# Optimization experiments

Measured on AMD Instinct MI355X. Metric: run time of the kernel, lower is better.

Reference implementation:

```python
import jax, jax.numpy as jnp
import numpy as np

P, N, M = 4, 8192, 8192

def setup_inputs() -> dict:
    key = jax.random.key(0)
    k1, k2, k3, k4, k5 = jax.random.split(key, 5)
    return {
        "camera_pts": jax.random.normal(k1, (P, N, 3), dtype=jnp.float32),
        "cad_pts": jax.random.normal(k2, (P, M, 3), dtype=jnp.float32),
        "part_weight": jax.random.uniform(k3, (P,), dtype=jnp.float32),
        "rot_quat": jax.random.normal(k4, (P, 4), dtype=jnp.float32),
        "tra": jax.random.normal(k5, (P, 3, 1), dtype=jnp.float32),
    }

def _quat_to_rot(q):
    # q: [P,4] in (w,x,y,z) order, normalized outside
    a, b, c, d = q[:, 0], q[:, 1], q[:, 2], q[:, 3]
    rows = jnp.stack([
        1 - 2*c*c - 2*d*d, 2*b*c - 2*a*d,     2*a*c + 2*b*d,
        2*b*c + 2*a*d,     1 - 2*b*b - 2*d*d, 2*c*d - 2*a*b,
        2*b*d - 2*a*c,     2*a*b + 2*c*d,     1 - 2*b*b - 2*c*c,
    ], axis=-1)  # [P,9]
    return rows.reshape(-1, 3, 3)

def _chamfer(x, y):
    # x: [N,4], y: [M,4] -> scalar bidirectional chamfer (Euclidean, not squared)
    x2 = jnp.sum(x * x, axis=-1)              # [N]
    y2 = jnp.sum(y * y, axis=-1)              # [M]
    d2 = x2[:, None] + y2[None, :] - 2.0 * (x @ y.T)
    dist = jnp.sqrt(jnp.clip(d2, 0.0))        # [N,M]
    return jnp.mean(jnp.min(dist, axis=1)) + jnp.mean(jnp.min(dist, axis=0))

def reference(camera_pts, cad_pts, part_weight, rot_quat, tra):
    q = rot_quat / jnp.linalg.norm(rot_quat, axis=1, keepdims=True)
    rot = _quat_to_rot(q)                                       # [P,3,3]
    top = jnp.concatenate([rot, tra], axis=2)                   # [P,3,4]
    bottom = jnp.broadcast_to(jnp.array([[[0.0, 0.0, 0.0, 1.0]]], dtype=rot.dtype), (rot.shape[0], 1, 4))
    transforms = jnp.concatenate([top, bottom], axis=1)         # [P,4,4]
    ones_cad = jnp.ones(cad_pts.shape[:-1] + (1,), dtype=cad_pts.dtype)
    ones_cam = jnp.ones(camera_pts.shape[:-1] + (1,), dtype=camera_pts.dtype)
    cad_h = jnp.concatenate([cad_pts, ones_cad], axis=-1)       # [P,M,4]
    cam_h = jnp.concatenate([camera_pts, ones_cam], axis=-1)    # [P,N,4]
    cad_base = jnp.einsum('pij,pmj->pmi', transforms, cad_h)    # [P,M,4]
    cd = jax.vmap(_chamfer)(cad_base, cam_h)                    # [P]
    all_objective = jnp.sum(part_weight * cd)
    return all_objective, jax.lax.stop_gradient(transforms)
```

## Files before the change

### kernel.cpp

```cpp
#include <hip/hip_runtime.h>
#include <math.h>

#define NP 4
#define NN 8192
#define NM 8192

#define PK_A_F4 0
#define PK_B_F4 (NP * NM)
#define MINS_OFF ((NP * NM + NP * NN) * 4)
#define MINB_REL (NP * NM)

#define TQ 16
#define QT 4096
#define SPLITS 64
#define SPAN 128

#define RED_BLOCKS 128

__device__ inline float min3f(float a, float b, float c) {
    float d;
    asm("v_min3_f32 %0, %1, %2, %3" : "=v"(d) : "v"(a), "v"(b), "v"(c));
    return d;
}

__device__ inline void make_transform(const float* __restrict__ quat,
                                      const float* __restrict__ tra,
                                      int p, float T[12]) {
    float q0 = quat[p * 4 + 0], q1 = quat[p * 4 + 1];
    float q2 = quat[p * 4 + 2], q3 = quat[p * 4 + 3];
    float inv = 1.0f / sqrtf(q0 * q0 + q1 * q1 + q2 * q2 + q3 * q3);
    float a = q0 * inv, b = q1 * inv, c = q2 * inv, d = q3 * inv;
    T[0] = 1.0f - 2.0f * c * c - 2.0f * d * d;
    T[1] = 2.0f * b * c - 2.0f * a * d;
    T[2] = 2.0f * a * c + 2.0f * b * d;
    T[3] = tra[p * 3 + 0];
    T[4] = 2.0f * b * c + 2.0f * a * d;
    T[5] = 1.0f - 2.0f * b * b - 2.0f * d * d;
    T[6] = 2.0f * c * d - 2.0f * a * b;
    T[7] = tra[p * 3 + 1];
    T[8] = 2.0f * b * d - 2.0f * a * c;
    T[9] = 2.0f * a * b + 2.0f * c * d;
    T[10] = 1.0f - 2.0f * b * b - 2.0f * c * c;
    T[11] = tra[p * 3 + 2];
}

__global__ __launch_bounds__(256) void prep_kernel(
    const float* __restrict__ cam, const float* __restrict__ cad,
    const float* __restrict__ quat, const float* __restrict__ tra,
    float* __restrict__ ws, float* __restrict__ out) {
    int idx = blockIdx.x * 256 + threadIdx.x;
    const float INF = __uint_as_float(0x7f800000u);

    if (idx < NP * NM) {
        int p = idx >> 13;
        int m = idx & (NM - 1);
        float T[12];
        make_transform(quat, tra, p, T);
        float x = cad[(p * NM + m) * 3 + 0];
        float y = cad[(p * NM + m) * 3 + 1];
        float z = cad[(p * NM + m) * 3 + 2];
        float vx = fmaf(T[0], x, fmaf(T[1], y, fmaf(T[2], z, T[3])));
        float vy = fmaf(T[4], x, fmaf(T[5], y, fmaf(T[6], z, T[7])));
        float vz = fmaf(T[8], x, fmaf(T[9], y, fmaf(T[10], z, T[11])));
        float h = 0.5f * (vx * vx + vy * vy + vz * vz);
        ((float4*)ws)[PK_A_F4 + idx] = make_float4(vx, vy, vz, h);
        ws[MINS_OFF + idx] = INF;
    } else {
        int k = idx - NP * NM;
        float vx = cam[k * 3 + 0];
        float vy = cam[k * 3 + 1];
        float vz = cam[k * 3 + 2];
        float h = 0.5f * (vx * vx + vy * vy + vz * vz);
        ((float4*)ws)[PK_B_F4 + k] = make_float4(vx, vy, vz, h);
        ws[MINS_OFF + MINB_REL + k] = INF;
    }

    if (idx < 64) {
        int p2 = idx >> 4;
        int r = (idx >> 2) & 3;
        int c = idx & 3;
        float T[12];
        make_transform(quat, tra, p2, T);
        float v;
        if (r == 3)
            v = (c == 3) ? 1.0f : 0.0f;
        else
            v = T[r * 4 + c];
        out[1 + idx] = v;
    } else if (idx == 64) {
        out[0] = 0.0f;
    }
}

__global__ __launch_bounds__(256, 2) void chamfer_kernel(
    const float4* __restrict__ packed, float* __restrict__ mins) {
    int tid = threadIdx.x;
    int p = blockIdx.z >> 1;
    int role = blockIdx.z & 1;

    const float4* Q;
    const float4* T;
    float* minarr;
    if (role == 0) {
        Q = packed + PK_A_F4 + p * NM;
        T = packed + PK_B_F4 + p * NN;
        minarr = mins + p * NM;
    } else {
        Q = packed + PK_B_F4 + p * NN;
        T = packed + PK_A_F4 + p * NM;
        minarr = mins + MINB_REL + p * NN;
    }

    __shared__ float4 sT[SPAN];

    const float INF = __uint_as_float(0x7f800000u);
    int q0 = blockIdx.x * QT + tid;
    float qx[TQ], qy[TQ], qz[TQ], qw[TQ], tmin[TQ];
#pragma unroll
    for (int k = 0; k < TQ; ++k) {
        float4 v = Q[q0 + k * 256];
        qx[k] = v.x; qy[k] = v.y; qz[k] = v.z; qw[k] = v.w;
        tmin[k] = INF;
    }

    int tbase = blockIdx.y * SPAN;
    for (int j = tid; j < SPAN; j += 256) sT[j] = T[tbase + j];
    __syncthreads();

#pragma unroll 2
    for (int j = 0; j < SPAN; j += 2) {
        float4 t0 = sT[j];
        float4 t1 = sT[j + 1];
#pragma unroll
        for (int k = 0; k < TQ; ++k) {
            float s0 = fmaf(-qx[k], t0.x, fmaf(-qy[k], t0.y, fmaf(-qz[k], t0.z, t0.w)));
            float s1 = fmaf(-qx[k], t1.x, fmaf(-qy[k], t1.y, fmaf(-qz[k], t1.z, t1.w)));
            tmin[k] = min3f(tmin[k], s0, s1);
        }
    }

#pragma unroll
    for (int k = 0; k < TQ; ++k) {
        float d2 = 2.0f * (qw[k] + tmin[k]);
        d2 = fmaxf(d2, 0.0f);
        atomicMin((unsigned int*)&minarr[q0 + k * 256], __float_as_uint(d2));
    }
}

__global__ __launch_bounds__(256) void finalize_kernel(
    const float* __restrict__ ws, const float* __restrict__ w,
    float* __restrict__ out) {
    const float* vals = ws + MINS_OFF;
    int i = blockIdx.x * 256 + threadIdx.x;
    int tid = threadIdx.x;

    float wl[4] = {w[0], w[1], w[2], w[3]};

    int i2 = i + 32768;
    float acc = wl[(i >> 13) & 3] * sqrtf(vals[i]) +
                wl[(i2 >> 13) & 3] * sqrtf(vals[i2]);

#pragma unroll
    for (int off = 32; off > 0; off >>= 1) acc += __shfl_down(acc, off, 64);

    __shared__ float wsum[4];
    if ((tid & 63) == 0) wsum[tid >> 6] = acc;
    __syncthreads();
    if (tid == 0) {
        float blocksum = (wsum[0] + wsum[1] + wsum[2] + wsum[3]) * (1.0f / 8192.0f);
        atomicAdd(out, blocksum);
    }
}

extern "C" void kernel_launch(void* const* d_in, const int* in_sizes, int n_in,
                              void* d_out, int out_size, void* d_ws, size_t ws_size,
                              hipStream_t stream) {
    const float* cam = (const float*)d_in[0];
    const float* cad = (const float*)d_in[1];
    const float* w = (const float*)d_in[2];
    const float* quat = (const float*)d_in[3];
    const float* tra = (const float*)d_in[4];
    float* out = (float*)d_out;
    float* ws = (float*)d_ws;

    prep_kernel<<<(NP * (NM + NN)) / 256, 256, 0, stream>>>(cam, cad, quat, tra, ws, out);

    dim3 grid(NM / QT, SPLITS, 2 * NP);
    chamfer_kernel<<<grid, 256, 0, stream>>>((const float4*)ws, ws + MINS_OFF);

    finalize_kernel<<<RED_BLOCKS, 256, 0, stream>>>(ws, w, out);
}
```

Measured before the change: 109.3 us.

## Use packed FP32 FMA with pair-interleaved target layout in chamfer kernel

Prep now also writes target points in a pair-interleaved SoA layout (x0x1,y0y1,z0z1,h0h1), so the chamfer inner loop can evaluate two targets per v_pk_fma_f32 and halve FMA instruction count. Queries per thread drop from 16 to 8 with more blocks, and launch bounds move to a waves-per-eu hint for higher occupancy. Shared-memory reads are software-prefetched one pair ahead. The risk is extra prep writes and larger grid/atomic traffic, plus relying on packed-math throughput.

```diff
diff --git a/kernel.cpp b/kernel.cpp
--- a/kernel.cpp
+++ b/kernel.cpp
@@ -5,21 +5,30 @@
 #define NN 8192
 #define NM 8192
 
-#define PK_A_F4 0
-#define PK_B_F4 (NP * NM)
-#define MINS_OFF ((NP * NM + NP * NN) * 4)
+#define PKA_OFF 0
+#define PKB_OFF 131072
+#define PRA_OFF 262144
+#define PRB_OFF 393216
+#define MINS_OFF 524288
 #define MINB_REL (NP * NM)
 
-#define TQ 16
-#define QT 4096
+#define TQ 8
+#define QT 2048
 #define SPLITS 64
 #define SPAN 128
 
-#define RED_BLOCKS 128
+typedef float float2v __attribute__((ext_vector_type(2)));
+typedef float float4v __attribute__((ext_vector_type(4)));
 
 __device__ inline float min3f(float a, float b, float c) {
     float d;
     asm("v_min3_f32 %0, %1, %2, %3" : "=v"(d) : "v"(a), "v"(b), "v"(c));
+    return d;
+}
+
+__device__ inline float2v pk_fma(float2v a, float2v b, float2v c) {
+    float2v d;
+    asm("v_pk_fma_f32 %0, %1, %2, %3" : "=v"(d) : "v"(a), "v"(b), "v"(c));
     return d;
 }
 
@@ -51,29 +60,40 @@
     int idx = blockIdx.x * 256 + threadIdx.x;
     const float INF = __uint_as_float(0x7f800000u);
 
+    float vx, vy, vz;
+    int pkoff, proff, local;
     if (idx < NP * NM) {
         int p = idx >> 13;
-        int m = idx & (NM - 1);
         float T[12];
         make_transform(quat, tra, p, T);
-        float x = cad[(p * NM + m) * 3 + 0];
-        float y = cad[(p * NM + m) * 3 + 1];
-        float z = cad[(p * NM + m) * 3 + 2];
-        float vx = fmaf(T[0], x, fmaf(T[1], y, fmaf(T[2], z, T[3])));
-        float vy = fmaf(T[4], x, fmaf(T[5], y, fmaf(T[6], z, T[7])));
-        float vz = fmaf(T[8], x, fmaf(T[9], y, fmaf(T[10], z, T[11])));
-        float h = 0.5f * (vx * vx + vy * vy + vz * vz);
-        ((float4*)ws)[PK_A_F4 + idx] = make_float4(vx, vy, vz, h);
-        ws[MINS_OFF + idx] = INF;
+        float x = cad[idx * 3 + 0];
+        float y = cad[idx * 3 + 1];
+        float z = cad[idx * 3 + 2];
+        vx = fmaf(T[0], x, fmaf(T[1], y, fmaf(T[2], z, T[3])));
+        vy = fmaf(T[4], x, fmaf(T[5], y, fmaf(T[6], z, T[7])));
+        vz = fmaf(T[8], x, fmaf(T[9], y, fmaf(T[10], z, T[11])));
+        pkoff = PKA_OFF;
+        proff = PRA_OFF;
+        local = idx;
     } else {
         int k = idx - NP * NM;
-        float vx = cam[k * 3 + 0];
-        float vy = cam[k * 3 + 1];
-        float vz = cam[k * 3 + 2];
-        float h = 0.5f * (vx * vx + vy * vy + vz * vz);
-        ((float4*)ws)[PK_B_F4 + k] = make_float4(vx, vy, vz, h);
-        ws[MINS_OFF + MINB_REL + k] = INF;
-    }
+        vx = cam[k * 3 + 0];
+        vy = cam[k * 3 + 1];
+        vz = cam[k * 3 + 2];
+        pkoff = PKB_OFF;
+        proff = PRB_OFF;
+        local = k;
+    }
+    float h = 0.5f * (vx * vx + vy * vy + vz * vz);
+    ((float4*)(ws + pkoff))[local] = make_float4(vx, vy, vz, h);
+    int lane = local & 1;
+    size_t f = (size_t)proff + (size_t)(local & ~1) * 4;
+    ws[f + lane] = vx;
+    ws[f + 2 + lane] = vy;
+    ws[f + 4 + lane] = vz;
+    ws[f + 6 + lane] = h;
+
+    ws[MINS_OFF + idx] = INF;
 
     if (idx < 64) {
         int p2 = idx >> 4;
@@ -92,51 +112,64 @@
     }
 }
 
-__global__ __launch_bounds__(256, 2) void chamfer_kernel(
-    const float4* __restrict__ packed, float* __restrict__ mins) {
+__global__ __launch_bounds__(256)
+__attribute__((amdgpu_waves_per_eu(2, 4)))
+void chamfer_kernel(const float* __restrict__ ws, float* __restrict__ mins) {
     int tid = threadIdx.x;
     int p = blockIdx.z >> 1;
     int role = blockIdx.z & 1;
 
     const float4* Q;
-    const float4* T;
+    const float4v* T;
     float* minarr;
     if (role == 0) {
-        Q = packed + PK_A_F4 + p * NM;
-        T = packed + PK_B_F4 + p * NN;
+        Q = (const float4*)(ws + PKA_OFF) + p * NM;
+        T = (const float4v*)(ws + PRB_OFF) + p * NN;
         minarr = mins + p * NM;
     } else {
-        Q = packed + PK_B_F4 + p * NN;
-        T = packed + PK_A_F4 + p * NM;
+        Q = (const float4*)(ws + PKB_OFF) + p * NN;
+        T = (const float4v*)(ws + PRA_OFF) + p * NM;
         minarr = mins + MINB_REL + p * NN;
     }
 
-    __shared__ float4 sT[SPAN];
+    __shared__ float4v sQd[SPAN];
 
     const float INF = __uint_as_float(0x7f800000u);
     int q0 = blockIdx.x * QT + tid;
-    float qx[TQ], qy[TQ], qz[TQ], qw[TQ], tmin[TQ];
+    float2v nqx[TQ], nqy[TQ], nqz[TQ];
+    float qw[TQ], tmin[TQ];
 #pragma unroll
     for (int k = 0; k < TQ; ++k) {
         float4 v = Q[q0 + k * 256];
-        qx[k] = v.x; qy[k] = v.y; qz[k] = v.z; qw[k] = v.w;
+        nqx[k] = (float2v){-v.x, -v.x};
+        nqy[k] = (float2v){-v.y, -v.y};
+        nqz[k] = (float2v){-v.z, -v.z};
+        qw[k] = v.w;
         tmin[k] = INF;
     }
 
     int tbase = blockIdx.y * SPAN;
-    for (int j = tid; j < SPAN; j += 256) sT[j] = T[tbase + j];
+    if (tid < SPAN) sQd[tid] = T[tbase + tid];
     __syncthreads();
 
+    float4v cXY = sQd[0], cZH = sQd[1];
 #pragma unroll 2
-    for (int j = 0; j < SPAN; j += 2) {
-        float4 t0 = sT[j];
-        float4 t1 = sT[j + 1];
+    for (int pp = 0; pp < SPAN / 2; ++pp) {
+        int pn = (pp + 1) & (SPAN / 2 - 1);
+        float4v nXY = sQd[2 * pn];
+        float4v nZH = sQd[2 * pn + 1];
+
+        float2v X = __builtin_shufflevector(cXY, cXY, 0, 1);
+        float2v Y = __builtin_shufflevector(cXY, cXY, 2, 3);
+        float2v Z = __builtin_shufflevector(cZH, cZH, 0, 1);
+        float2v H = __builtin_shufflevector(cZH, cZH, 2, 3);
 #pragma unroll
         for (int k = 0; k < TQ; ++k) {
-            float s0 = fmaf(-qx[k], t0.x, fmaf(-qy[k], t0.y, fmaf(-qz[k], t0.z, t0.w)));
-            float s1 = fmaf(-qx[k], t1.x, fmaf(-qy[k], t1.y, fmaf(-qz[k], t1.z, t1.w)));
-            tmin[k] = min3f(tmin[k], s0, s1);
+            float2v s = pk_fma(nqx[k], X, pk_fma(nqy[k], Y, pk_fma(nqz[k], Z, H)));
+            tmin[k] = min3f(tmin[k], s.x, s.y);
         }
+        cXY = nXY;
+        cZH = nZH;
     }
 
 #pragma unroll
@@ -183,10 +216,10 @@
     float* out = (float*)d_out;
     float* ws = (float*)d_ws;
 
-    prep_kernel<<<(NP * (NM + NN)) / 256, 256, 0, stream>>>(cam, cad, quat, tra, ws, out);
+    prep_kernel<<<256, 256, 0, stream>>>(cam, cad, quat, tra, ws, out);
 
     dim3 grid(NM / QT, SPLITS, 2 * NP);
-    chamfer_kernel<<<grid, 256, 0, stream>>>((const float4*)ws, ws + MINS_OFF);
-
-    finalize_kernel<<<RED_BLOCKS, 256, 0, stream>>>(ws, w, out);
-}
+    chamfer_kernel<<<grid, 256, 0, stream>>>(ws, ws + MINS_OFF);
+
+    finalize_kernel<<<128, 256, 0, stream>>>(ws, w, out);
+}
```

New measurement: 104.8 us. -4.1%, faster.

## Compute both chamfer directions in one pass with packed FMA and DPP reductions

Applied to the files above, without the earlier changes.

Replaces the two-role chamfer pass, which evaluated every distance twice, with a single pass per point pair that updates both the per-camera-point minimum in registers and the per-CAD-point minimum via a wave-level DPP min reduction. The prep kernel is fused into the chamfer kernel, and the global atomicMin is replaced by partial-minimum buffers that the finalize kernel reduces. Distance evaluation uses v_pk_fma_f32 on pairs of target points, and a bias term folds the second half-norm in with a single packed add. The cost is extra DPP/readlane work for each query point, a larger workspace for the partial minima, and a heavier finalize reduction over 64 slices.

```diff
diff --git a/kernel.cpp b/kernel.cpp
--- a/kernel.cpp
+++ b/kernel.cpp
@@ -5,23 +5,38 @@
 #define NN 8192
 #define NM 8192
 
-#define PK_A_F4 0
-#define PK_B_F4 (NP * NM)
-#define MINS_OFF ((NP * NM + NP * NN) * 4)
-#define MINB_REL (NP * NM)
-
-#define TQ 16
-#define QT 4096
-#define SPLITS 64
-#define SPAN 128
-
-#define RED_BLOCKS 128
+#define QS 64
+#define QB 128
+#define TS 2
+#define TT 16
+#define SLAB 4096
+
+#define BIAS 1024.0f
+
+#define PA_OFF 0
+#define PB_OFF (TS * NP * NM)
+
+typedef float float2v __attribute__((ext_vector_type(2)));
 
 __device__ inline float min3f(float a, float b, float c) {
     float d;
     asm("v_min3_f32 %0, %1, %2, %3" : "=v"(d) : "v"(a), "v"(b), "v"(c));
     return d;
 }
+__device__ inline float2v pk_fma(float2v a, float2v b, float2v c) {
+    float2v d;
+    asm("v_pk_fma_f32 %0, %1, %2, %3" : "=v"(d) : "v"(a), "v"(b), "v"(c));
+    return d;
+}
+__device__ inline float2v pk_add(float2v a, float2v b) {
+    float2v d;
+    asm("v_pk_add_f32 %0, %1, %2" : "=v"(d) : "v"(a), "v"(b));
+    return d;
+}
+
+#define DPP_MIN(r, ctrl)                                                     \
+    r = fminf(r, __uint_as_float((unsigned)__builtin_amdgcn_update_dpp(      \
+                     0, (int)__float_as_uint(r), (ctrl), 0xf, 0xf, true)))
 
 __device__ inline void make_transform(const float* __restrict__ quat,
                                       const float* __restrict__ tra,
@@ -44,121 +59,117 @@
     T[11] = tra[p * 3 + 2];
 }
 
-__global__ __launch_bounds__(256) void prep_kernel(
+__global__ __launch_bounds__(256, 2) void chamfer_kernel(
     const float* __restrict__ cam, const float* __restrict__ cad,
     const float* __restrict__ quat, const float* __restrict__ tra,
     float* __restrict__ ws, float* __restrict__ out) {
-    int idx = blockIdx.x * 256 + threadIdx.x;
+    int tid = threadIdx.x;
+    int lane = tid & 63;
+    int wv = tid >> 6;
+    int qb = blockIdx.x;
+    int ts = blockIdx.y;
+    int p = blockIdx.z;
     const float INF = __uint_as_float(0x7f800000u);
 
-    if (idx < NP * NM) {
-        int p = idx >> 13;
-        int m = idx & (NM - 1);
+    __shared__ float4 sQ[QB];
+    __shared__ float sMA[4 * QB];
+
+    if (tid < QB) {
         float T[12];
         make_transform(quat, tra, p, T);
-        float x = cad[(p * NM + m) * 3 + 0];
-        float y = cad[(p * NM + m) * 3 + 1];
-        float z = cad[(p * NM + m) * 3 + 2];
+        int g = p * NM + qb * QB + tid;
+        float x = cad[g * 3 + 0], y = cad[g * 3 + 1], z = cad[g * 3 + 2];
         float vx = fmaf(T[0], x, fmaf(T[1], y, fmaf(T[2], z, T[3])));
         float vy = fmaf(T[4], x, fmaf(T[5], y, fmaf(T[6], z, T[7])));
         float vz = fmaf(T[8], x, fmaf(T[9], y, fmaf(T[10], z, T[11])));
         float h = 0.5f * (vx * vx + vy * vy + vz * vz);
-        ((float4*)ws)[PK_A_F4 + idx] = make_float4(vx, vy, vz, h);
-        ws[MINS_OFF + idx] = INF;
-    } else {
-        int k = idx - NP * NM;
-        float vx = cam[k * 3 + 0];
-        float vy = cam[k * 3 + 1];
-        float vz = cam[k * 3 + 2];
-        float h = 0.5f * (vx * vx + vy * vy + vz * vz);
-        ((float4*)ws)[PK_B_F4 + k] = make_float4(vx, vy, vz, h);
-        ws[MINS_OFF + MINB_REL + k] = INF;
-    }
-
-    if (idx < 64) {
-        int p2 = idx >> 4;
-        int r = (idx >> 2) & 3;
-        int c = idx & 3;
-        float T[12];
-        make_transform(quat, tra, p2, T);
-        float v;
-        if (r == 3)
-            v = (c == 3) ? 1.0f : 0.0f;
-        else
-            v = T[r * 4 + c];
-        out[1 + idx] = v;
-    } else if (idx == 64) {
-        out[0] = 0.0f;
-    }
-}
-
-__global__ __launch_bounds__(256, 2) void chamfer_kernel(
-    const float4* __restrict__ packed, float* __restrict__ mins) {
-    int tid = threadIdx.x;
-    int p = blockIdx.z >> 1;
-    int role = blockIdx.z & 1;
-
-    const float4* Q;
-    const float4* T;
-    float* minarr;
-    if (role == 0) {
-        Q = packed + PK_A_F4 + p * NM;
-        T = packed + PK_B_F4 + p * NN;
-        minarr = mins + p * NM;
-    } else {
-        Q = packed + PK_B_F4 + p * NN;
-        T = packed + PK_A_F4 + p * NM;
-        minarr = mins + MINB_REL + p * NN;
-    }
-
-    __shared__ float4 sT[SPAN];
-
-    const float INF = __uint_as_float(0x7f800000u);
-    int q0 = blockIdx.x * QT + tid;
-    float qx[TQ], qy[TQ], qz[TQ], qw[TQ], tmin[TQ];
-#pragma unroll
-    for (int k = 0; k < TQ; ++k) {
-        float4 v = Q[q0 + k * 256];
-        qx[k] = v.x; qy[k] = v.y; qz[k] = v.z; qw[k] = v.w;
-        tmin[k] = INF;
-    }
-
-    int tbase = blockIdx.y * SPAN;
-    for (int j = tid; j < SPAN; j += 256) sT[j] = T[tbase + j];
+        sQ[tid] = make_float4(-vx, -vy, -vz, h);
+    } else if (qb == 0 && ts == 0 && p == 0) {
+        int t2 = tid - QB;
+        if (t2 < 64) {
+            int p2 = t2 >> 4, r = (t2 >> 2) & 3, c = t2 & 3;
+            float T[12];
+            make_transform(quat, tra, p2, T);
+            out[1 + t2] = (r == 3) ? ((c == 3) ? 1.0f : 0.0f) : T[r * 4 + c];
+        } else if (t2 == 64) {
+            out[0] = 0.0f;
+        }
+    }
+
+    float2v TX[TT / 2], TY[TT / 2], TZ[TT / 2], THb[TT / 2];
+    float fminB[TT];
+#pragma unroll
+    for (int j = 0; j < TT; ++j) {
+        int n = ts * SLAB + j * 256 + tid;
+        int g = p * NN + n;
+        float bx = cam[g * 3 + 0], by = cam[g * 3 + 1], bz = cam[g * 3 + 2];
+        float hb = 0.5f * (bx * bx + by * by + bz * bz);
+        TX[j >> 1][j & 1] = bx;
+        TY[j >> 1][j & 1] = by;
+        TZ[j >> 1][j & 1] = bz;
+        THb[j >> 1][j & 1] = hb - BIAS;
+        fminB[j] = INF;
+    }
     __syncthreads();
 
 #pragma unroll 2
-    for (int j = 0; j < SPAN; j += 2) {
-        float4 t0 = sT[j];
-        float4 t1 = sT[j + 1];
-#pragma unroll
-        for (int k = 0; k < TQ; ++k) {
-            float s0 = fmaf(-qx[k], t0.x, fmaf(-qy[k], t0.y, fmaf(-qz[k], t0.z, t0.w)));
-            float s1 = fmaf(-qx[k], t1.x, fmaf(-qy[k], t1.y, fmaf(-qz[k], t1.z, t1.w)));
-            tmin[k] = min3f(tmin[k], s0, s1);
+    for (int q = 0; q < QB; ++q) {
+        float4 qv = sQ[q];
+        float2v nx = {qv.x, qv.x};
+        float2v ny = {qv.y, qv.y};
+        float2v nz = {qv.z, qv.z};
+        float2v ah = {qv.w, qv.w};
+        float m = 0.0f;
+#pragma unroll
+        for (int i = 0; i < TT / 2; ++i) {
+            float2v u = pk_fma(nx, TX[i], pk_fma(ny, TY[i], pk_fma(nz, TZ[i], ah)));
+            fminB[2 * i] = fminf(fminB[2 * i], u[0]);
+            fminB[2 * i + 1] = fminf(fminB[2 * i + 1], u[1]);
+            float2v wb = pk_add(u, THb[i]);
+            m = min3f(m, wb[0], wb[1]);
         }
-    }
-
-#pragma unroll
-    for (int k = 0; k < TQ; ++k) {
-        float d2 = 2.0f * (qw[k] + tmin[k]);
-        d2 = fmaxf(d2, 0.0f);
-        atomicMin((unsigned int*)&minarr[q0 + k * 256], __float_as_uint(d2));
+        DPP_MIN(m, 0x111);
+        DPP_MIN(m, 0x112);
+        DPP_MIN(m, 0x114);
+        DPP_MIN(m, 0x118);
+        DPP_MIN(m, 0x142);
+        DPP_MIN(m, 0x143);
+        float red = __uint_as_float(
+            (unsigned)__builtin_amdgcn_readlane(__float_as_uint(m), 63));
+        if (lane == 0) sMA[wv * QB + q] = red;
+    }
+    __syncthreads();
+
+    if (tid < QB) {
+        float va = fminf(fminf(sMA[tid], sMA[QB + tid]),
+                         fminf(sMA[2 * QB + tid], sMA[3 * QB + tid]));
+        ws[PA_OFF + ts * (NP * NM) + p * NM + qb * QB + tid] = va + BIAS;
+    }
+#pragma unroll
+    for (int j = 0; j < TT; ++j) {
+        int n = ts * SLAB + j * 256 + tid;
+        float hb = THb[j >> 1][j & 1] + BIAS;
+        ws[PB_OFF + qb * (NP * NN) + p * NN + n] = fminB[j] + hb;
     }
 }
 
 __global__ __launch_bounds__(256) void finalize_kernel(
     const float* __restrict__ ws, const float* __restrict__ w,
     float* __restrict__ out) {
-    const float* vals = ws + MINS_OFF;
     int i = blockIdx.x * 256 + threadIdx.x;
     int tid = threadIdx.x;
-
-    float wl[4] = {w[0], w[1], w[2], w[3]};
-
-    int i2 = i + 32768;
-    float acc = wl[(i >> 13) & 3] * sqrtf(vals[i]) +
-                wl[(i2 >> 13) & 3] * sqrtf(vals[i2]);
+    const float INF = __uint_as_float(0x7f800000u);
+
+    float va = INF;
+#pragma unroll
+    for (int s = 0; s < TS; ++s) va = fminf(va, ws[PA_OFF + s * (NP * NM) + i]);
+    float vb = INF;
+#pragma unroll 8
+    for (int s = 0; s < QS; ++s) vb = fminf(vb, ws[PB_OFF + s * (NP * NN) + i]);
+
+    float wp = w[(i >> 13) & 3];
+    float acc = wp * (sqrtf(fmaxf(2.0f * va, 0.0f)) +
+                      sqrtf(fmaxf(2.0f * vb, 0.0f)));
 
 #pragma unroll
     for (int off = 32; off > 0; off >>= 1) acc += __shfl_down(acc, off, 64);
@@ -183,10 +194,8 @@
     float* out = (float*)d_out;
     float* ws = (float*)d_ws;
 
-    prep_kernel<<<(NP * (NM + NN)) / 256, 256, 0, stream>>>(cam, cad, quat, tra, ws, out);
-
-    dim3 grid(NM / QT, SPLITS, 2 * NP);
-    chamfer_kernel<<<grid, 256, 0, stream>>>((const float4*)ws, ws + MINS_OFF);
-
-    finalize_kernel<<<RED_BLOCKS, 256, 0, stream>>>(ws, w, out);
-}
+    dim3 grid(QS, TS, NP);
+    chamfer_kernel<<<grid, 256, 0, stream>>>(cam, cad, quat, tra, ws, out);
+
+    finalize_kernel<<<128, 256, 0, stream>>>(ws, w, out);
+}
```

Result: slower. 122.8 us (+12.4%).
